# Kernel tuning notes

Hardware: AMD Instinct MI355X
Metric: run time of the kernel (lower is better)

The kernel has to match this reference:

```python
import jax, jax.numpy as jnp
import numpy as np

B, S, D, H = 2, 2048, 1024, 16
DK = D // H  # 64
THETA = 10000.0
SCALE = 1.0 / np.sqrt(DK)


def _rope(t, pos):
    """Apply rotary embedding. t: [b,h,s,dk], pos: [b,s] int."""
    inv_freq = THETA ** (-jnp.arange(0, DK, 2, dtype=jnp.float32) / DK)  # [dk/2]
    ang = pos[:, None, :, None].astype(jnp.float32) * inv_freq  # [b,1,s,dk/2]
    cos, sin = jnp.cos(ang), jnp.sin(ang)
    t1, t2 = t[..., 0::2], t[..., 1::2]  # interleaved pairs
    rot = jnp.stack([t1 * cos - t2 * sin, t1 * sin + t2 * cos], axis=-1)
    return rot.reshape(t.shape)


def setup_inputs() -> dict:
    key = jax.random.key(0)
    ks = jax.random.split(key, 9)
    sc = 0.02
    x = jax.random.normal(ks[0], (B, S, D), jnp.float32)
    token_position = jnp.tile(jnp.arange(S, dtype=jnp.int32)[None, :], (B, 1))
    Wq = jax.random.normal(ks[1], (D, D), jnp.float32) * sc
    Wk = jax.random.normal(ks[2], (D, D), jnp.float32) * sc
    Wv = jax.random.normal(ks[3], (D, D), jnp.float32) * sc
    Wo = jax.random.normal(ks[4], (D, D), jnp.float32) * sc
    bq = jnp.zeros((D,), jnp.float32)
    bk = jnp.zeros((D,), jnp.float32)
    bv = jnp.zeros((D,), jnp.float32)
    bo = jnp.zeros((D,), jnp.float32)
    return {"x": x, "token_position": token_position,
            "Wq": Wq, "bq": bq, "Wk": Wk, "bk": bk,
            "Wv": Wv, "bv": bv, "Wo": Wo, "bo": bo}


def reference(x, token_position, Wq, bq, Wk, bk, Wv, bv, Wo, bo):
    b, s, d = x.shape
    # projections, split heads: [b,s,d] -> [b,h,s,dk]
    def heads(t):
        return t.reshape(b, s, H, DK).transpose(0, 2, 1, 3)
    q = heads(x @ Wq + bq)
    k = heads(x @ Wk + bk)
    v = heads(x @ Wv + bv)
    q = _rope(q, token_position)
    k = _rope(k, token_position)
    scores = jnp.einsum('bhnk,bhmk->bhnm', q, k) * SCALE  # [b,h,s,s]
    causal = jnp.tril(jnp.ones((s, s), dtype=bool))
    scores = jnp.where(causal, scores, -jnp.inf)
    probs = jax.nn.softmax(scores, axis=-1)
    o = jnp.einsum('bhnm,bhmk->bhnk', probs, v)  # [b,h,s,dk]
    o = o.transpose(0, 2, 1, 3).reshape(b, s, d)
    return o @ Wo + bo
```

## Files before the change

kernel.cpp:

```cpp
#include <hip/hip_runtime.h>
#include <math.h>

#define BB  2
#define SS  2048
#define DD  1024
#define HH  16
#define DKK 64

constexpr float kScale = 0.125f;
constexpr float kC1 = 0.18033688011112042f;
constexpr float kC2 = 23.0831206542234144f;

typedef __bf16 bf16x8 __attribute__((ext_vector_type(8)));
typedef __bf16 bf16x4 __attribute__((ext_vector_type(4)));
typedef float f32x4 __attribute__((ext_vector_type(4)));

__device__ __forceinline__ void async_copy16(const void* g, void* l) {
  __builtin_amdgcn_global_load_lds(
      (const __attribute__((address_space(1))) void*)g,
      (__attribute__((address_space(3))) void*)l, 16, 0, 0);
}

__global__ __launch_bounds__(256) void prep_kernel(
    const float* __restrict__ x, const int* __restrict__ pos,
    const float* __restrict__ W0, const float* __restrict__ W1,
    const float* __restrict__ W2, const float* __restrict__ W3,
    __bf16* __restrict__ xb, float2* __restrict__ rtab,
    __bf16* __restrict__ T0, __bf16* __restrict__ T1,
    __bf16* __restrict__ T2, __bf16* __restrict__ T3) {
  __shared__ __bf16 tile[64][65];
  const int bid = blockIdx.x;
  const int t = threadIdx.x;
  if (bid < 2048) {
    const size_t i = ((size_t)bid * 256 + t) * 8;
    const float4 v0 = *(const float4*)(x + i);
    const float4 v1 = *(const float4*)(x + i + 4);
    bf16x8 o;
    o[0] = (__bf16)v0.x; o[1] = (__bf16)v0.y; o[2] = (__bf16)v0.z; o[3] = (__bf16)v0.w;
    o[4] = (__bf16)v1.x; o[5] = (__bf16)v1.y; o[6] = (__bf16)v1.z; o[7] = (__bf16)v1.w;
    *(bf16x8*)(xb + i) = o;
  } else if (bid < 2560) {
    const int idx = (bid - 2048) * 256 + t;
    const int m = idx >> 5, pi = idx & 31;
    const float inv = exp2f(-0.4152410118609203f * (float)pi);
    float sn, cs;
    __sincosf((float)pos[m] * inv, &sn, &cs);
    rtab[idx] = make_float2(cs, sn);
  } else {
    const int tid2 = bid - 2560;
    const int z = tid2 >> 8, rem = tid2 & 255;
    const float* W;
    __bf16* T;
    switch (z) {
      case 0: W = W0; T = T0; break;
      case 1: W = W1; T = T1; break;
      case 2: W = W2; T = T2; break;
      default: W = W3; T = T3; break;
    }
    const int k0 = (rem >> 4) * 64, n0 = (rem & 15) * 64;
    const int c = t & 63, rg = t >> 6;
#pragma unroll
    for (int i = 0; i < 16; i++) {
      const int r = rg + i * 4;
      tile[r][c] = (__bf16)W[(size_t)(k0 + r) * DD + n0 + c];
    }
    __syncthreads();
#pragma unroll
    for (int i = 0; i < 16; i++) {
      const int r = rg + i * 4;
      T[(size_t)(n0 + r) * DD + k0 + c] = tile[c][r];
    }
  }
}

__device__ __forceinline__ void gemm_core(
    const __bf16* __restrict__ A, const __bf16* __restrict__ Bt,
    int bm, int bn, f32x4 (&acc)[4][4], __bf16* As, __bf16* Bs) {
  const int t = threadIdx.x;
  const int lane = t & 63, wave = t >> 6;
  const int col = lane & 15, quad = lane >> 4;
  const int wm = (wave & 1) * 64, wn = (wave >> 1) * 64;
  const int r8 = lane >> 3;
  const int cg = (lane & 7) ^ r8;
  const __bf16* ag = A + (size_t)(bm + wave * 32 + r8) * DD + cg * 8;
  const __bf16* bg = Bt + (size_t)(bn + wave * 32 + r8) * DD + cg * 8;
  __bf16* asb = As + wave * 32 * 64;
  __bf16* bsb = Bs + wave * 32 * 64;

  for (int kt = 0; kt < DD; kt += 64) {
#pragma unroll
    for (int c = 0; c < 4; c++) {
      async_copy16(ag + (size_t)c * 8 * DD + kt, asb + c * 512);
      async_copy16(bg + (size_t)c * 8 * DD + kt, bsb + c * 512);
    }
    __syncthreads();
#pragma unroll
    for (int ks = 0; ks < 2; ks++) {
      bf16x8 af[4], bf[4];
#pragma unroll
      for (int i = 0; i < 4; i++)
        af[i] = *(const bf16x8*)(As + (wm + i * 16 + col) * 64 +
                                 (((ks * 4 + quad) ^ (col & 7)) * 8));
#pragma unroll
      for (int j = 0; j < 4; j++)
        bf[j] = *(const bf16x8*)(Bs + (wn + j * 16 + col) * 64 +
                                 (((ks * 4 + quad) ^ (col & 7)) * 8));
#pragma unroll
      for (int i = 0; i < 4; i++)
#pragma unroll
        for (int j = 0; j < 4; j++)
          acc[i][j] =
              __builtin_amdgcn_mfma_f32_16x16x32_bf16(af[i], bf[j], acc[i][j], 0, 0, 0);
    }
    __syncthreads();
  }
}

__global__ __launch_bounds__(256) void qkv_gemm_kernel(
    const __bf16* __restrict__ xb, const __bf16* __restrict__ WqT,
    const __bf16* __restrict__ WkT, const __bf16* __restrict__ WvT,
    const float* __restrict__ bq, const float* __restrict__ bk,
    const float* __restrict__ bv, const float2* __restrict__ ropetab,
    __bf16* __restrict__ qo, __bf16* __restrict__ ko, __bf16* __restrict__ vo) {
  __shared__ __bf16 As[128 * 64];
  __shared__ __bf16 Bs[128 * 64];
  const int mat = blockIdx.x >> 3;
  const int bn = (blockIdx.x & 7) * 128;
  const int bm = blockIdx.y * 128;

  f32x4 acc[4][4] = {};
  const int t = threadIdx.x, lane = t & 63, wave = t >> 6;
  const int col = lane & 15, quad = lane >> 4;
  const int wm = (wave & 1) * 64, wn = (wave >> 1) * 64;

  if (mat == 2) {
    gemm_core(WvT, xb, bn, bm, acc, As, Bs);
    const int b = bm >> 11;
#pragma unroll
    for (int i = 0; i < 4; i++) {
#pragma unroll
      for (int r = 0; r < 4; r++) {
        const int n = bn + wm + i * 16 + quad * 4 + r;
        const float bb = bv[n];
        const int h = n >> 6, dk = n & 63;
        __bf16* vrow = vo + ((size_t)(b * HH + h) * DKK + dk) * SS;
#pragma unroll
        for (int j = 0; j < 4; j++) {
          const int m = bm + wn + j * 16 + col;
          vrow[m & (SS - 1)] = (__bf16)(acc[i][j][r] + bb);
        }
      }
    }
    return;
  }

  const __bf16* Bt = mat == 0 ? WqT : WkT;
  const float* bias = mat == 0 ? bq : bk;
  __bf16* out = mat == 0 ? qo : ko;
  gemm_core(xb, Bt, bm, bn, acc, As, Bs);

#pragma unroll
  for (int i = 0; i < 4; i++) {
#pragma unroll
    for (int j = 0; j < 4; j++) {
      const int n = bn + wn + j * 16 + col;
      const float bb = bias[n];
      const int pi = (n & 63) >> 1;
#pragma unroll
      for (int r = 0; r < 4; r++) {
        const int m = bm + wm + i * 16 + quad * 4 + r;
        float v = acc[i][j][r] + bb;
        {
          const float other = __shfl_xor(v, 1, 64);
          const float2 cssn = ropetab[(size_t)m * 32 + pi];
          v = (n & 1) ? (other * cssn.y + v * cssn.x)
                      : (v * cssn.x - other * cssn.y);
        }
        const int h = n >> 6, dk = n & 63;
        const int b = m >> 11, s = m & (SS - 1);
        out[((size_t)(b * HH + h) * SS + s) * DKK + dk] = (__bf16)v;
      }
    }
  }
}

__global__ __launch_bounds__(256) void oproj_gemm_kernel(
    const __bf16* __restrict__ ob, const __bf16* __restrict__ WoT,
    const float* __restrict__ bo, float* __restrict__ out) {
  __shared__ __bf16 As[128 * 64];
  __shared__ __bf16 Bs[128 * 64];
  const int bn = blockIdx.x * 128;
  const int bm = blockIdx.y * 128;
  f32x4 acc[4][4] = {};
  gemm_core(ob, WoT, bm, bn, acc, As, Bs);

  const int t = threadIdx.x, lane = t & 63, wave = t >> 6;
  const int col = lane & 15, quad = lane >> 4;
  const int wm = (wave & 1) * 64, wn = (wave >> 1) * 64;
#pragma unroll
  for (int i = 0; i < 4; i++) {
#pragma unroll
    for (int j = 0; j < 4; j++) {
      const int n = bn + wn + j * 16 + col;
      const float bb = bo[n];
#pragma unroll
      for (int r = 0; r < 4; r++) {
        const int m = bm + wm + i * 16 + quad * 4 + r;
        out[(size_t)m * DD + n] = acc[i][j][r] + bb;
      }
    }
  }
}

__global__ __launch_bounds__(256) void flash_attn_mfma_kernel(
    const __bf16* __restrict__ q, const __bf16* __restrict__ k,
    const __bf16* __restrict__ vt, __bf16* __restrict__ o) {
  __shared__ __bf16 Ks[2][64 * 64];
  __shared__ __bf16 Vs[2][64 * 64];
  __shared__ __bf16 Ps[4][16 * 72];

  const int bh = blockIdx.x;
  const int qt = 31 - blockIdx.y;
  const int t = threadIdx.x, lane = t & 63, wave = t >> 6;
  const int col = lane & 15, quad = lane >> 4;
  const int r8 = lane >> 3;
  const int cg = (lane & 7) ^ r8;

  const __bf16* qb = q + (size_t)bh * SS * DKK;
  const __bf16* kb = k + (size_t)bh * SS * DKK;
  const __bf16* vtb = vt + (size_t)bh * DKK * SS;
  const int b = bh / HH, h = bh % HH;
  __bf16* pw = (__bf16*)Ps[wave];

  const int rbase = qt * 64 + wave * 16;

  bf16x8 qf[2];
#pragma unroll
  for (int ks = 0; ks < 2; ks++)
    qf[ks] = *(const bf16x8*)(qb + (size_t)(rbase + col) * DKK + ks * 32 +
                              quad * 8);

  f32x4 oacc[4] = {};
  float l_lane = 0.f;

  auto stage = [&](int kt, int buf) {
#pragma unroll
    for (int i = 0; i < 2; i++) {
      const int slab = wave * 2 + i;
      async_copy16(kb + (size_t)(kt * 64 + slab * 8 + r8) * DKK + cg * 8,
                   &Ks[buf][slab * 512]);
      async_copy16(vtb + (size_t)(slab * 8 + r8) * SS + kt * 64 + cg * 8,
                   &Vs[buf][slab * 512]);
    }
  };

  stage(0, 0);
  __syncthreads();

  int cur = 0;
  for (int kt = 0; kt <= qt; kt++) {
    if (kt < qt) stage(kt + 1, cur ^ 1);

    f32x4 sc[4] = {};
    __builtin_amdgcn_s_setprio(1);
#pragma unroll
    for (int ct = 0; ct < 4; ct++)
#pragma unroll
      for (int ks = 0; ks < 2; ks++) {
        const bf16x8 kf = *(const bf16x8*)(&Ks[cur][(ct * 16 + col) * 64 +
                                           (((ks * 4 + quad) ^ (col & 7)) * 8)]);
        sc[ct] = __builtin_amdgcn_mfma_f32_16x16x32_bf16(kf, qf[ks], sc[ct],
                                                         0, 0, 0);
      }
    __builtin_amdgcn_s_setprio(0);

    if (kt < qt) {
#pragma unroll
      for (int ct = 0; ct < 4; ct++) {
        float p0 = exp2f(sc[ct][0] * kC1 - kC2);
        float p1 = exp2f(sc[ct][1] * kC1 - kC2);
        float p2 = exp2f(sc[ct][2] * kC1 - kC2);
        float p3 = exp2f(sc[ct][3] * kC1 - kC2);
        l_lane += (p0 + p1) + (p2 + p3);
        bf16x4 pv;
        pv[0] = (__bf16)p0; pv[1] = (__bf16)p1;
        pv[2] = (__bf16)p2; pv[3] = (__bf16)p3;
        *(bf16x4*)(pw + col * 72 + ct * 16 + quad * 4) = pv;
      }
    } else {
#pragma unroll
      for (int ct = 0; ct < 4; ct++) {
        bf16x4 pv;
        if (ct > wave) {
          pv[0] = pv[1] = pv[2] = pv[3] = (__bf16)0.0f;
        } else if (ct < wave) {
          float p0 = exp2f(sc[ct][0] * kC1 - kC2);
          float p1 = exp2f(sc[ct][1] * kC1 - kC2);
          float p2 = exp2f(sc[ct][2] * kC1 - kC2);
          float p3 = exp2f(sc[ct][3] * kC1 - kC2);
          l_lane += (p0 + p1) + (p2 + p3);
          pv[0] = (__bf16)p0; pv[1] = (__bf16)p1;
          pv[2] = (__bf16)p2; pv[3] = (__bf16)p3;
        } else {
#pragma unroll
          for (int r = 0; r < 4; r++) {
            float p = exp2f(sc[ct][r] * kC1 - kC2);
            if (ct * 16 + quad * 4 + r > wave * 16 + col) p = 0.0f;
            l_lane += p;
            pv[r] = (__bf16)p;
          }
        }
        *(bf16x4*)(pw + col * 72 + ct * 16 + quad * 4) = pv;
      }
    }

    {
      bf16x8 pf[2];
#pragma unroll
      for (int ks = 0; ks < 2; ks++)
        pf[ks] = *(const bf16x8*)(pw + col * 72 + ks * 32 + quad * 8);
      __builtin_amdgcn_s_setprio(1);
#pragma unroll
      for (int dt = 0; dt < 4; dt++)
#pragma unroll
        for (int ks = 0; ks < 2; ks++) {
          const bf16x8 vf = *(const bf16x8*)(&Vs[cur][(dt * 16 + col) * 64 +
                                             (((ks * 4 + quad) ^ (col & 7)) * 8)]);
          oacc[dt] = __builtin_amdgcn_mfma_f32_16x16x32_bf16(pf[ks], vf,
                                                             oacc[dt], 0, 0, 0);
        }
      __builtin_amdgcn_s_setprio(0);
    }

    __syncthreads();
    cur ^= 1;
  }

  float l = l_lane;
  l += __shfl_xor(l, 16, 64);
  l += __shfl_xor(l, 32, 64);
#pragma unroll
  for (int r = 0; r < 4; r++) {
    const float lr = __shfl(l, quad * 4 + r, 64);
    const float inv_l = 1.0f / lr;
    const int s = rbase + quad * 4 + r;
#pragma unroll
    for (int dt = 0; dt < 4; dt++)
      o[((size_t)(b * SS + s) * HH + h) * DKK + dt * 16 + col] =
          (__bf16)(oacc[dt][r] * inv_l);
  }
}

extern "C" void kernel_launch(void* const* d_in, const int* in_sizes, int n_in,
                              void* d_out, int out_size, void* d_ws,
                              size_t ws_size, hipStream_t stream) {
  const float* x  = (const float*)d_in[0];
  const int*  pos = (const int*)d_in[1];
  const float* Wq = (const float*)d_in[2];
  const float* bq = (const float*)d_in[3];
  const float* Wk = (const float*)d_in[4];
  const float* bk = (const float*)d_in[5];
  const float* Wv = (const float*)d_in[6];
  const float* bv = (const float*)d_in[7];
  const float* Wo = (const float*)d_in[8];
  const float* bo = (const float*)d_in[9];
  float* out = (float*)d_out;

  char* ws = (char*)d_ws;
  __bf16* xb  = (__bf16*)(ws);
  __bf16* WqT = (__bf16*)(ws + ((size_t)8  << 20));
  __bf16* WkT = (__bf16*)(ws + ((size_t)10 << 20));
  __bf16* WvT = (__bf16*)(ws + ((size_t)12 << 20));
  __bf16* WoT = (__bf16*)(ws + ((size_t)14 << 20));
  __bf16* qb  = (__bf16*)(ws + ((size_t)16 << 20));
  __bf16* kb  = (__bf16*)(ws + ((size_t)24 << 20));
  __bf16* vtb = (__bf16*)(ws + ((size_t)32 << 20));
  __bf16* ob  = (__bf16*)(ws + ((size_t)40 << 20));
  float2* rtab = (float2*)(ws + ((size_t)48 << 20));

  prep_kernel<<<3584, 256, 0, stream>>>(x, pos, Wq, Wk, Wv, Wo, xb, rtab, WqT,
                                        WkT, WvT, WoT);
  qkv_gemm_kernel<<<dim3(24, 32), 256, 0, stream>>>(xb, WqT, WkT, WvT, bq, bk,
                                                    bv, rtab, qb, kb, vtb);
  flash_attn_mfma_kernel<<<dim3(32, 32), 256, 0, stream>>>(qb, kb, vtb, ob);
  oproj_gemm_kernel<<<dim3(8, 32), 256, 0, stream>>>(ob, WoT, bo, out);
}
```

Measured before the change: 196.2 us.

## Enlarge flash-attention query tile to 128 rows with 8 waves sharing K/V

Each attention block now handles 128 query rows with 8 waves instead of 64 rows with 4. Every staged 64-key K/V tile is reused by twice as many waves, which halves global K/V traffic and the staging work per wave, since each wave now issues one async copy per tile. Waves in the first half of the block skip the final K tile because it lies past their diagonal, but they still take part in the barrier. The trade-off is a grid of half the size with more idle waves at the diagonal, and 512-thread blocks that may lower occupancy.

```diff
diff --git a/kernel.cpp b/kernel.cpp
--- a/kernel.cpp
+++ b/kernel.cpp
@@ -212,19 +212,20 @@
   }
 }
 
-__global__ __launch_bounds__(256) void flash_attn_mfma_kernel(
+__global__ __launch_bounds__(512, 4) void flash_attn_mfma_kernel(
     const __bf16* __restrict__ q, const __bf16* __restrict__ k,
     const __bf16* __restrict__ vt, __bf16* __restrict__ o) {
   __shared__ __bf16 Ks[2][64 * 64];
   __shared__ __bf16 Vs[2][64 * 64];
-  __shared__ __bf16 Ps[4][16 * 72];
+  __shared__ __bf16 Ps[8][16 * 72];
 
   const int bh = blockIdx.x;
-  const int qt = 31 - blockIdx.y;
+  const int qtile = 15 - blockIdx.y;
   const int t = threadIdx.x, lane = t & 63, wave = t >> 6;
   const int col = lane & 15, quad = lane >> 4;
   const int r8 = lane >> 3;
   const int cg = (lane & 7) ^ r8;
+  const int w4 = wave & 3;
 
   const __bf16* qb = q + (size_t)bh * SS * DKK;
   const __bf16* kb = k + (size_t)bh * SS * DKK;
@@ -232,7 +233,9 @@
   const int b = bh / HH, h = bh % HH;
   __bf16* pw = (__bf16*)Ps[wave];
 
-  const int rbase = qt * 64 + wave * 16;
+  const int rbase = qtile * 128 + wave * 16;
+  const int myDiag = 2 * qtile + (wave >> 2);
+  const int nTiles = 2 * qtile + 2;
 
   bf16x8 qf[2];
 #pragma unroll
@@ -244,92 +247,90 @@
   float l_lane = 0.f;
 
   auto stage = [&](int kt, int buf) {
-#pragma unroll
-    for (int i = 0; i < 2; i++) {
-      const int slab = wave * 2 + i;
-      async_copy16(kb + (size_t)(kt * 64 + slab * 8 + r8) * DKK + cg * 8,
-                   &Ks[buf][slab * 512]);
-      async_copy16(vtb + (size_t)(slab * 8 + r8) * SS + kt * 64 + cg * 8,
-                   &Vs[buf][slab * 512]);
-    }
+    async_copy16(kb + (size_t)(kt * 64 + wave * 8 + r8) * DKK + cg * 8,
+                 &Ks[buf][wave * 512]);
+    async_copy16(vtb + (size_t)(wave * 8 + r8) * SS + kt * 64 + cg * 8,
+                 &Vs[buf][wave * 512]);
   };
 
   stage(0, 0);
   __syncthreads();
 
   int cur = 0;
-  for (int kt = 0; kt <= qt; kt++) {
-    if (kt < qt) stage(kt + 1, cur ^ 1);
-
-    f32x4 sc[4] = {};
-    __builtin_amdgcn_s_setprio(1);
-#pragma unroll
-    for (int ct = 0; ct < 4; ct++)
-#pragma unroll
-      for (int ks = 0; ks < 2; ks++) {
-        const bf16x8 kf = *(const bf16x8*)(&Ks[cur][(ct * 16 + col) * 64 +
-                                           (((ks * 4 + quad) ^ (col & 7)) * 8)]);
-        sc[ct] = __builtin_amdgcn_mfma_f32_16x16x32_bf16(kf, qf[ks], sc[ct],
-                                                         0, 0, 0);
-      }
-    __builtin_amdgcn_s_setprio(0);
-
-    if (kt < qt) {
-#pragma unroll
-      for (int ct = 0; ct < 4; ct++) {
-        float p0 = exp2f(sc[ct][0] * kC1 - kC2);
-        float p1 = exp2f(sc[ct][1] * kC1 - kC2);
-        float p2 = exp2f(sc[ct][2] * kC1 - kC2);
-        float p3 = exp2f(sc[ct][3] * kC1 - kC2);
-        l_lane += (p0 + p1) + (p2 + p3);
-        bf16x4 pv;
-        pv[0] = (__bf16)p0; pv[1] = (__bf16)p1;
-        pv[2] = (__bf16)p2; pv[3] = (__bf16)p3;
-        *(bf16x4*)(pw + col * 72 + ct * 16 + quad * 4) = pv;
-      }
-    } else {
-#pragma unroll
-      for (int ct = 0; ct < 4; ct++) {
-        bf16x4 pv;
-        if (ct > wave) {
-          pv[0] = pv[1] = pv[2] = pv[3] = (__bf16)0.0f;
-        } else if (ct < wave) {
+  for (int kt = 0; kt < nTiles; kt++) {
+    if (kt + 1 < nTiles) stage(kt + 1, cur ^ 1);
+
+    if (kt <= myDiag) {
+      f32x4 sc[4] = {};
+      __builtin_amdgcn_s_setprio(1);
+#pragma unroll
+      for (int ct = 0; ct < 4; ct++)
+#pragma unroll
+        for (int ks = 0; ks < 2; ks++) {
+          const bf16x8 kf = *(const bf16x8*)(&Ks[cur][(ct * 16 + col) * 64 +
+                                             (((ks * 4 + quad) ^ (col & 7)) * 8)]);
+          sc[ct] = __builtin_amdgcn_mfma_f32_16x16x32_bf16(kf, qf[ks], sc[ct],
+                                                           0, 0, 0);
+        }
+      __builtin_amdgcn_s_setprio(0);
+
+      if (kt < myDiag) {
+#pragma unroll
+        for (int ct = 0; ct < 4; ct++) {
           float p0 = exp2f(sc[ct][0] * kC1 - kC2);
           float p1 = exp2f(sc[ct][1] * kC1 - kC2);
           float p2 = exp2f(sc[ct][2] * kC1 - kC2);
           float p3 = exp2f(sc[ct][3] * kC1 - kC2);
           l_lane += (p0 + p1) + (p2 + p3);
+          bf16x4 pv;
           pv[0] = (__bf16)p0; pv[1] = (__bf16)p1;
           pv[2] = (__bf16)p2; pv[3] = (__bf16)p3;
-        } else {
-#pragma unroll
-          for (int r = 0; r < 4; r++) {
-            float p = exp2f(sc[ct][r] * kC1 - kC2);
-            if (ct * 16 + quad * 4 + r > wave * 16 + col) p = 0.0f;
-            l_lane += p;
-            pv[r] = (__bf16)p;
+          *(bf16x4*)(pw + col * 72 + ct * 16 + quad * 4) = pv;
+        }
+      } else {
+#pragma unroll
+        for (int ct = 0; ct < 4; ct++) {
+          bf16x4 pv;
+          if (ct > w4) {
+            pv[0] = pv[1] = pv[2] = pv[3] = (__bf16)0.0f;
+          } else if (ct < w4) {
+            float p0 = exp2f(sc[ct][0] * kC1 - kC2);
+            float p1 = exp2f(sc[ct][1] * kC1 - kC2);
+            float p2 = exp2f(sc[ct][2] * kC1 - kC2);
+            float p3 = exp2f(sc[ct][3] * kC1 - kC2);
+            l_lane += (p0 + p1) + (p2 + p3);
+            pv[0] = (__bf16)p0; pv[1] = (__bf16)p1;
+            pv[2] = (__bf16)p2; pv[3] = (__bf16)p3;
+          } else {
+#pragma unroll
+            for (int r = 0; r < 4; r++) {
+              float p = exp2f(sc[ct][r] * kC1 - kC2);
+              if (quad * 4 + r > col) p = 0.0f;
+              l_lane += p;
+              pv[r] = (__bf16)p;
+            }
           }
-        }
-        *(bf16x4*)(pw + col * 72 + ct * 16 + quad * 4) = pv;
-      }
-    }
-
-    {
-      bf16x8 pf[2];
-#pragma unroll
-      for (int ks = 0; ks < 2; ks++)
-        pf[ks] = *(const bf16x8*)(pw + col * 72 + ks * 32 + quad * 8);
-      __builtin_amdgcn_s_setprio(1);
-#pragma unroll
-      for (int dt = 0; dt < 4; dt++)
-#pragma unroll
-        for (int ks = 0; ks < 2; ks++) {
-          const bf16x8 vf = *(const bf16x8*)(&Vs[cur][(dt * 16 + col) * 64 +
-                                             (((ks * 4 + quad) ^ (col & 7)) * 8)]);
-          oacc[dt] = __builtin_amdgcn_mfma_f32_16x16x32_bf16(pf[ks], vf,
-                                                             oacc[dt], 0, 0, 0);
-        }
-      __builtin_amdgcn_s_setprio(0);
+          *(bf16x4*)(pw + col * 72 + ct * 16 + quad * 4) = pv;
+        }
+      }
+
+      {
+        bf16x8 pf[2];
+#pragma unroll
+        for (int ks = 0; ks < 2; ks++)
+          pf[ks] = *(const bf16x8*)(pw + col * 72 + ks * 32 + quad * 8);
+        __builtin_amdgcn_s_setprio(1);
+#pragma unroll
+        for (int dt = 0; dt < 4; dt++)
+#pragma unroll
+          for (int ks = 0; ks < 2; ks++) {
+            const bf16x8 vf = *(const bf16x8*)(&Vs[cur][(dt * 16 + col) * 64 +
+                                               (((ks * 4 + quad) ^ (col & 7)) * 8)]);
+            oacc[dt] = __builtin_amdgcn_mfma_f32_16x16x32_bf16(pf[ks], vf,
+                                                               oacc[dt], 0, 0, 0);
+          }
+        __builtin_amdgcn_s_setprio(0);
+      }
     }
 
     __syncthreads();
@@ -382,6 +383,6 @@
                                         WkT, WvT, WoT);
   qkv_gemm_kernel<<<dim3(24, 32), 256, 0, stream>>>(xb, WqT, WkT, WvT, bq, bk,
                                                     bv, rtab, qb, kb, vtb);
-  flash_attn_mfma_kernel<<<dim3(32, 32), 256, 0, stream>>>(qb, kb, vtb, ob);
+  flash_attn_mfma_kernel<<<dim3(32, 16), 512, 0, stream>>>(qb, kb, vtb, ob);
   oproj_gemm_kernel<<<dim3(8, 32), 256, 0, stream>>>(ob, WoT, bo, out);
 }
```

Result: no change. 199.1 us (+1.5%).
